# Kernel optimization log

Measured on AMD Instinct MI355X. Metric: run time of the kernel, lower is better.

## Reference

```python
import jax, jax.numpy as jnp
import numpy as np

K = 9          # kernel_size
PAD = 4        # padding
N_OUT, C_IN = 32, 32


def setup_inputs() -> dict:
    key = jax.random.key(0)
    k1, k2, k3, k4, k5 = jax.random.split(key, 5)
    x = jax.random.normal(k1, (16, C_IN, 192, 192), jnp.float32)
    sx = jax.random.uniform(k2, (N_OUT, C_IN), jnp.float32, 0.2, 4.0)
    sy = jax.random.uniform(k3, (N_OUT, C_IN), jnp.float32, 0.2, 4.0)
    th = jax.random.uniform(k4, (N_OUT, C_IN), jnp.float32, 0.0, 2.0 * np.pi)
    weight = jnp.stack([sx, sy, th], axis=-1)          # [N, C, 3]
    bias = jax.random.normal(k5, (N_OUT,), jnp.float32) * 0.01
    return {"x": x, "weight": weight, "bias": bias}


def _gaussian_kernels(weight, k):
    # weight: [N, C, 3] -> normalized anisotropic Gaussian kernels [N, C, k, k]
    sx, sy = weight[..., 0], weight[..., 1]
    rad = weight[..., 2] / 180.0 * jnp.pi          # matches theta/180*pi in source
    c, s = jnp.cos(rad), jnp.sin(rad)
    sx2, sy2 = sx * sx, sy * sy
    # Sigma = U diag(sx^2, sy^2) U^T, U = [[c,-s],[s,c]] -> Sigma = [[a,b],[b,d]]
    a = c * c * sx2 + s * s * sy2
    b = c * s * (sx2 - sy2)
    d = s * s * sx2 + c * c * sy2
    det = a * d - b * b
    ia, ib, id_ = d / det, -b / det, a / det       # closed-form 2x2 inverse
    ax = jnp.arange(k, dtype=jnp.float32) - k // 2
    xx = ax[None, :]                               # x varies along columns
    yy = ax[:, None]                               # y varies along rows
    # quadratic form: ia*x^2 + 2*ib*x*y + id*y^2, broadcast to [N, C, k, k]
    q = (ia[..., None, None] * (xx * xx)
         + 2.0 * ib[..., None, None] * (xx * yy)
         + id_[..., None, None] * (yy * yy))
    ker = jnp.exp(-0.5 * q)
    return ker / jnp.sum(ker, axis=(-2, -1), keepdims=True)


def reference(x, weight, bias):
    w = _gaussian_kernels(weight, K)               # [N, C, K, K]
    out = jax.lax.conv_general_dilated(
        x, w, window_strides=(1, 1), padding=[(PAD, PAD), (PAD, PAD)],
        dimension_numbers=("NCHW", "OIHW", "NCHW"))
    return out + bias[None, :, None, None]
```

## Files before the change

kernel.cpp:

```cpp
#include <hip/hip_runtime.h>
#include <stdint.h>

#define H 192
#define W 192
#define CIN 32
#define NOUT 32
#define NB 16
#define PADI 4

#define HT 16
#define WTL 16
#define RROWS 24
#define RCOLS 24

typedef __attribute__((ext_vector_type(8))) short bf16x8;
typedef __attribute__((ext_vector_type(4))) float f32x4;

__device__ __forceinline__ unsigned short f2bf(float f) {
    union { float f; unsigned int u; } v; v.f = f;
    unsigned int r = v.u + 0x7fffu + ((v.u >> 16) & 1u);
    return (unsigned short)(r >> 16);
}

__device__ __forceinline__ unsigned int cvtpk_bf16(float lo, float hi) {
    unsigned int r;
    asm("v_cvt_pk_bf16_f32 %0, %1, %2" : "=v"(r) : "v"(lo), "v"(hi));
    return r;
}

__global__ void genw_kernel(const float* __restrict__ wp, unsigned short* __restrict__ W2g) {
    const int b = blockIdx.x;
    const int o = b >> 5;
    const int i = b & 31;
    const int t = threadIdx.x;

    float sx = wp[b * 3 + 0], sy = wp[b * 3 + 1], th = wp[b * 3 + 2];
    float rad = th / 180.0f * 3.14159265358979323846f;
    float co = cosf(rad), si = sinf(rad);
    float sx2 = sx * sx, sy2 = sy * sy;
    float a = co * co * sx2 + si * si * sy2;
    float bb = co * si * (sx2 - sy2);
    float d = si * si * sx2 + co * co * sy2;
    float det = a * d - bb * bb;
    float ia = d / det, ib = -bb / det, idd = a / det;

    const int tap = t;
    float e = 0.0f;
    if (tap < 81) {
        float xx = (float)(tap % 9 - 4);
        float yy = (float)(tap / 9 - 4);
        float q = ia * xx * xx + 2.0f * ib * xx * yy + idd * yy * yy;
        e = expf(-0.5f * q);
    }
    float s = e;
    #pragma unroll
    for (int off = 32; off > 0; off >>= 1) s += __shfl_down(s, off);
    __shared__ float ws[2];
    if ((t & 63) == 0) ws[t >> 6] = s;
    __syncthreads();
    float total = ws[0] + ws[1];

    if (tap < 81) {
        int mt = o >> 4, m = o & 15, quad = i >> 3, j = i & 7;
        W2g[((((mt * 81 + tap) * 4 + quad) * 16 + m) << 3) + j] = f2bf(e / total);
    }
}

__global__ __launch_bounds__(256, 4) void conv_kernel(
    const float* __restrict__ x, const unsigned short* __restrict__ W2g,
    const float* __restrict__ bias, float* __restrict__ out)
{
    __shared__ __align__(16) unsigned short ldsx[4 * RROWS * RCOLS * 8];

    const int t = threadIdx.x;
    const int bid = (blockIdx.x & 7) * 288 + (blockIdx.x >> 3);
    const int wb = bid % (W / WTL);
    const int hb = (bid / (W / WTL)) % (H / HT);
    const int n  = bid / ((W / WTL) * (H / HT));
    const int row0 = hb * HT - PADI;
    const int col0 = wb * WTL - PADI;
    const float* xn = x + (size_t)n * CIN * H * W;

    const int wave = t >> 6;
    const int lane = t & 63;
    const int l15 = lane & 15;
    const int quad4 = lane >> 4;
    const int mt = wave & 1;
    const int rbase = (wave >> 1) * 8;

    float bb[4];
    #pragma unroll
    for (int reg = 0; reg < 4; reg++) bb[reg] = bias[mt * 16 + quad4 * 4 + reg];

    float v[9][8];
    #pragma unroll
    for (int it = 0; it < 9; ++it) {
        int idx = it * 256 + t;
        int w = idx % RCOLS;
        int r = (idx / RCOLS) % RROWS;
        int quad = idx / (RCOLS * RROWS);
        int row = row0 + r, col = col0 + w;
        #pragma unroll
        for (int k = 0; k < 8; k++) v[it][k] = 0.0f;
        if ((unsigned)row < (unsigned)H && (unsigned)col < (unsigned)W) {
            const float* p = xn + ((size_t)(quad * 8) * H + row) * W + col;
            #pragma unroll
            for (int k = 0; k < 8; k++) v[it][k] = p[(size_t)k * H * W];
        }
    }
    #pragma unroll
    for (int it = 0; it < 9; ++it) {
        int idx = it * 256 + t;
        unsigned int d[4];
        #pragma unroll
        for (int k = 0; k < 4; k++)
            d[k] = cvtpk_bf16(v[it][2 * k], v[it][2 * k + 1]);
        *(uint4*)&ldsx[(size_t)idx * 8] = make_uint4(d[0], d[1], d[2], d[3]);
    }

    const bf16x8* __restrict__ Wpt = (const bf16x8*)W2g;

    bf16x8 A[2][9];
    #pragma unroll
    for (int dy = 0; dy < 9; dy++)
        A[0][dy] = Wpt[((mt * 81 + dy * 9 + 0) * 4 + quad4) * 16 + l15];

    __syncthreads();

    f32x4 acc[8];
    #pragma unroll
    for (int i = 0; i < 8; i++)
        acc[i] = (f32x4){bb[0], bb[1], bb[2], bb[3]};

    const unsigned short* bptr = &ldsx[(size_t)(((quad4 * RROWS + rbase) * RCOLS) + l15) * 8];

    #pragma unroll
    for (int dx = 0; dx < 9; dx++) {
        const int cur = dx & 1, nxt = cur ^ 1;
        if (dx < 8) {
            #pragma unroll
            for (int dy = 0; dy < 9; dy++)
                A[nxt][dy] = Wpt[((mt * 81 + dy * 9 + (dx + 1)) * 4 + quad4) * 16 + l15];
        }
        #pragma unroll
        for (int rr = 0; rr < 16; rr++) {
            const bf16x8 bfrag = *(const bf16x8*)&bptr[(size_t)(rr * RCOLS + dx) * 8];
            #pragma unroll
            for (int dy = 0; dy < 9; dy++) {
                const int orr = rr - dy;
                if (orr >= 0 && orr < 8) {
                    acc[orr] = __builtin_amdgcn_mfma_f32_16x16x32_bf16(
                        A[cur][dy], bfrag, acc[orr], 0, 0, 0);
                }
            }
        }
    }

    float* outn = out + (size_t)n * NOUT * H * W;
    #pragma unroll
    for (int orr = 0; orr < 8; orr++) {
        const int row = hb * HT + rbase + orr;
        const int col = wb * WTL + l15;
        #pragma unroll
        for (int reg = 0; reg < 4; reg++) {
            const int och = mt * 16 + quad4 * 4 + reg;
            outn[((size_t)och * H + row) * W + col] = acc[orr][reg];
        }
    }
}

extern "C" void kernel_launch(void* const* d_in, const int* in_sizes, int n_in,
                              void* d_out, int out_size, void* d_ws, size_t ws_size,
                              hipStream_t stream) {
    const float* x    = (const float*)d_in[0];
    const float* wp   = (const float*)d_in[1];
    const float* bias = (const float*)d_in[2];
    float* out = (float*)d_out;
    unsigned short* W2g = (unsigned short*)d_ws;

    genw_kernel<<<NOUT * CIN, 128, 0, stream>>>(wp, W2g);
    const int blocks = NB * (H / HT) * (W / WTL);
    conv_kernel<<<blocks, 256, 0, stream>>>(x, W2g, bias, out);
}
```

Measured before the change: 188.4 us.

## Widen conv tile to 32 columns, each wave computing both output-channel halves

The spatial tile width is doubled to 32 columns. Each wave now computes all 32 output channels (two accumulator sets) for a 16-column half instead of one 16-channel half, so each LDS B-fragment feeds two MFMAs. This shrinks halo overhead (a 40-column halo for 32 outputs instead of 24 for 16) and halves the number of blocks. Weight prefetch is ping-ponged with explicit buffers and MFMA sections get raised wave priority. The cost is about twice the accumulator and weight registers, with launch bounds lowered to 2 blocks per CU, so occupancy drops.

Result: no change. 189.0 us (+0.3%).

```diff
diff --git a/kernel.cpp b/kernel.cpp
--- a/kernel.cpp
+++ b/kernel.cpp
@@ -9,9 +9,10 @@
 #define PADI 4
 
 #define HT 16
-#define WTL 16
-#define RROWS 24
-#define RCOLS 24
+#define WT2 32
+#define RR2 24
+#define RC2 40
+#define NT (NB * (H / HT) * (W / WT2))
 
 typedef __attribute__((ext_vector_type(8))) short bf16x8;
 typedef __attribute__((ext_vector_type(4))) float f32x4;
@@ -66,39 +67,42 @@
     }
 }
 
-__global__ __launch_bounds__(256, 4) void conv_kernel(
+__global__ __launch_bounds__(256, 2) void conv_kernel(
     const float* __restrict__ x, const unsigned short* __restrict__ W2g,
     const float* __restrict__ bias, float* __restrict__ out)
 {
-    __shared__ __align__(16) unsigned short ldsx[4 * RROWS * RCOLS * 8];
+    __shared__ __align__(16) unsigned short ldsx[4 * RR2 * RC2 * 8];
 
     const int t = threadIdx.x;
-    const int bid = (blockIdx.x & 7) * 288 + (blockIdx.x >> 3);
-    const int wb = bid % (W / WTL);
-    const int hb = (bid / (W / WTL)) % (H / HT);
-    const int n  = bid / ((W / WTL) * (H / HT));
+    const int bid = (blockIdx.x & 7) * 144 + (blockIdx.x >> 3);
+    const int wb = bid % (W / WT2);
+    const int hb = (bid / (W / WT2)) % (H / HT);
+    const int n  = bid / ((W / WT2) * (H / HT));
     const int row0 = hb * HT - PADI;
-    const int col0 = wb * WTL - PADI;
+    const int col0 = wb * WT2 - PADI;
     const float* xn = x + (size_t)n * CIN * H * W;
 
     const int wave = t >> 6;
     const int lane = t & 63;
     const int l15 = lane & 15;
     const int quad4 = lane >> 4;
-    const int mt = wave & 1;
+    const int ch2 = wave & 1;
     const int rbase = (wave >> 1) * 8;
 
-    float bb[4];
-    #pragma unroll
-    for (int reg = 0; reg < 4; reg++) bb[reg] = bias[mt * 16 + quad4 * 4 + reg];
-
-    float v[9][8];
-    #pragma unroll
-    for (int it = 0; it < 9; ++it) {
+    float bb0[4], bb1[4];
+    #pragma unroll
+    for (int reg = 0; reg < 4; reg++) {
+        bb0[reg] = bias[quad4 * 4 + reg];
+        bb1[reg] = bias[16 + quad4 * 4 + reg];
+    }
+
+    float v[15][8];
+    #pragma unroll
+    for (int it = 0; it < 15; ++it) {
         int idx = it * 256 + t;
-        int w = idx % RCOLS;
-        int r = (idx / RCOLS) % RROWS;
-        int quad = idx / (RCOLS * RROWS);
+        int w = idx % RC2;
+        int r = (idx / RC2) % RR2;
+        int quad = idx / (RC2 * RR2);
         int row = row0 + r, col = col0 + w;
         #pragma unroll
         for (int k = 0; k < 8; k++) v[it][k] = 0.0f;
@@ -109,7 +113,7 @@
         }
     }
     #pragma unroll
-    for (int it = 0; it < 9; ++it) {
+    for (int it = 0; it < 15; ++it) {
         int idx = it * 256 + t;
         unsigned int d[4];
         #pragma unroll
@@ -120,51 +124,69 @@
 
     const bf16x8* __restrict__ Wpt = (const bf16x8*)W2g;
 
-    bf16x8 A[2][9];
-    #pragma unroll
-    for (int dy = 0; dy < 9; dy++)
-        A[0][dy] = Wpt[((mt * 81 + dy * 9 + 0) * 4 + quad4) * 16 + l15];
+    bf16x8 Aa0[9], Aa1[9], Ab0[9], Ab1[9];
+    #pragma unroll
+    for (int dy = 0; dy < 9; dy++) {
+        Aa0[dy] = Wpt[((dy * 9 + 0) * 4 + quad4) * 16 + l15];
+        Aa1[dy] = Wpt[((81 + dy * 9 + 0) * 4 + quad4) * 16 + l15];
+    }
 
     __syncthreads();
 
-    f32x4 acc[8];
-    #pragma unroll
-    for (int i = 0; i < 8; i++)
-        acc[i] = (f32x4){bb[0], bb[1], bb[2], bb[3]};
-
-    const unsigned short* bptr = &ldsx[(size_t)(((quad4 * RROWS + rbase) * RCOLS) + l15) * 8];
-
-    #pragma unroll
-    for (int dx = 0; dx < 9; dx++) {
-        const int cur = dx & 1, nxt = cur ^ 1;
-        if (dx < 8) {
-            #pragma unroll
-            for (int dy = 0; dy < 9; dy++)
-                A[nxt][dy] = Wpt[((mt * 81 + dy * 9 + (dx + 1)) * 4 + quad4) * 16 + l15];
-        }
-        #pragma unroll
-        for (int rr = 0; rr < 16; rr++) {
-            const bf16x8 bfrag = *(const bf16x8*)&bptr[(size_t)(rr * RCOLS + dx) * 8];
-            #pragma unroll
-            for (int dy = 0; dy < 9; dy++) {
-                const int orr = rr - dy;
-                if (orr >= 0 && orr < 8) {
-                    acc[orr] = __builtin_amdgcn_mfma_f32_16x16x32_bf16(
-                        A[cur][dy], bfrag, acc[orr], 0, 0, 0);
-                }
-            }
-        }
-    }
+    f32x4 acc0[8], acc1[8];
+    #pragma unroll
+    for (int i = 0; i < 8; i++) {
+        acc0[i] = (f32x4){bb0[0], bb0[1], bb0[2], bb0[3]};
+        acc1[i] = (f32x4){bb1[0], bb1[1], bb1[2], bb1[3]};
+    }
+
+    const unsigned short* bptr =
+        &ldsx[(size_t)(((quad4 * RR2 + rbase) * RC2) + ch2 * 16 + l15) * 8];
+
+#define DX_BODY(Ac0, Ac1, An0, An1, dxv, pfv, DO_PF)                          \
+    {                                                                          \
+        if (DO_PF) {                                                           \
+            _Pragma("unroll")                                                  \
+            for (int dy = 0; dy < 9; dy++) {                                   \
+                An0[dy] = Wpt[((dy * 9 + (pfv)) * 4 + quad4) * 16 + l15];      \
+                An1[dy] = Wpt[((81 + dy * 9 + (pfv)) * 4 + quad4) * 16 + l15]; \
+            }                                                                  \
+        }                                                                      \
+        __builtin_amdgcn_s_setprio(1);                                         \
+        _Pragma("unroll")                                                      \
+        for (int rr = 0; rr < 16; rr++) {                                      \
+            const bf16x8 bfrag =                                               \
+                *(const bf16x8*)&bptr[(size_t)(rr * RC2 + (dxv)) * 8];         \
+            _Pragma("unroll")                                                  \
+            for (int dy = 0; dy < 9; dy++) {                                   \
+                const int orr = rr - dy;                                       \
+                if (orr >= 0 && orr < 8) {                                     \
+                    acc0[orr] = __builtin_amdgcn_mfma_f32_16x16x32_bf16(       \
+                        Ac0[dy], bfrag, acc0[orr], 0, 0, 0);                   \
+                    acc1[orr] = __builtin_amdgcn_mfma_f32_16x16x32_bf16(       \
+                        Ac1[dy], bfrag, acc1[orr], 0, 0, 0);                   \
+                }                                                              \
+            }                                                                  \
+        }                                                                      \
+        __builtin_amdgcn_s_setprio(0);                                         \
+    }
+
+    for (int dx = 0; dx < 8; dx += 2) {
+        DX_BODY(Aa0, Aa1, Ab0, Ab1, dx, dx + 1, true);
+        DX_BODY(Ab0, Ab1, Aa0, Aa1, dx + 1, dx + 2, true);
+    }
+    DX_BODY(Aa0, Aa1, Ab0, Ab1, 8, 0, false);
+#undef DX_BODY
 
     float* outn = out + (size_t)n * NOUT * H * W;
+    const int col = wb * WT2 + ch2 * 16 + l15;
     #pragma unroll
     for (int orr = 0; orr < 8; orr++) {
         const int row = hb * HT + rbase + orr;
-        const int col = wb * WTL + l15;
         #pragma unroll
         for (int reg = 0; reg < 4; reg++) {
-            const int och = mt * 16 + quad4 * 4 + reg;
-            outn[((size_t)och * H + row) * W + col] = acc[orr][reg];
+            outn[((size_t)(quad4 * 4 + reg) * H + row) * W + col] = acc0[orr][reg];
+            outn[((size_t)(16 + quad4 * 4 + reg) * H + row) * W + col] = acc1[orr][reg];
         }
     }
 }
@@ -179,6 +201,5 @@
     unsigned short* W2g = (unsigned short*)d_ws;
 
     genw_kernel<<<NOUT * CIN, 128, 0, stream>>>(wp, W2g);
-    const int blocks = NB * (H / HT) * (W / WTL);
-    conv_kernel<<<blocks, 256, 0, stream>>>(x, W2g, bias, out);
-}
+    conv_kernel<<<NT, 256, 0, stream>>>(x, W2g, bias, out);
+}
```

## Make conv kernel persistent with register-staged prefetch of next tile

Applied to the files above, without the earlier changes.

Replaces the one-tile-per-block grid with a persistent grid of 512 blocks, each handling 4-5 consecutive tiles within one XCD's range. The global loads for the next tile are issued into registers after the LDS sync, so they overlap the current tile's MFMA work. MFMA sections also raise wave priority via s_setprio, and the launch bound drops to 2 blocks per CU. The volatile pointer on x forces loads to be issued in order and stops the compiler from moving them. This may limit scheduling, and the lower occupancy and extra register pressure could cost more than the overlap gains.

After: 396.1 us. 110% more time.

```diff
diff --git a/kernel.cpp b/kernel.cpp
--- a/kernel.cpp
+++ b/kernel.cpp
@@ -12,6 +12,9 @@
 #define WTL 16
 #define RROWS 24
 #define RCOLS 24
+#define NTILES (NB * (H / HT) * (W / WTL))
+#define NBLK 512
+#define TPX (NTILES / 8)
 
 typedef __attribute__((ext_vector_type(8))) short bf16x8;
 typedef __attribute__((ext_vector_type(4))) float f32x4;
@@ -66,20 +69,18 @@
     }
 }
 
-__global__ __launch_bounds__(256, 4) void conv_kernel(
+__global__ __launch_bounds__(256, 2) void conv_kernel(
     const float* __restrict__ x, const unsigned short* __restrict__ W2g,
     const float* __restrict__ bias, float* __restrict__ out)
 {
     __shared__ __align__(16) unsigned short ldsx[4 * RROWS * RCOLS * 8];
 
     const int t = threadIdx.x;
-    const int bid = (blockIdx.x & 7) * 288 + (blockIdx.x >> 3);
-    const int wb = bid % (W / WTL);
-    const int hb = (bid / (W / WTL)) % (H / HT);
-    const int n  = bid / ((W / WTL) * (H / HT));
-    const int row0 = hb * HT - PADI;
-    const int col0 = wb * WTL - PADI;
-    const float* xn = x + (size_t)n * CIN * H * W;
+    const int xcd  = blockIdx.x & 7;
+    const int slot = blockIdx.x >> 3;
+    int t0, cnt;
+    if (slot < 32) { cnt = 5; t0 = xcd * TPX + slot * 5; }
+    else           { cnt = 4; t0 = xcd * TPX + 160 + (slot - 32) * 4; }
 
     const int wave = t >> 6;
     const int lane = t & 63;
@@ -88,85 +89,114 @@
     const int mt = wave & 1;
     const int rbase = (wave >> 1) * 8;
 
+    int gw[9], gr[9], gq[9];
+    #pragma unroll
+    for (int it = 0; it < 9; ++it) {
+        const int idx = it * 256 + t;
+        gw[it] = idx % RCOLS;
+        gr[it] = (idx / RCOLS) % RROWS;
+        gq[it] = idx / (RCOLS * RROWS);
+    }
+
+    const bf16x8* __restrict__ Wpt = (const bf16x8*)W2g;
     float bb[4];
     #pragma unroll
     for (int reg = 0; reg < 4; reg++) bb[reg] = bias[mt * 16 + quad4 * 4 + reg];
 
+    const volatile float* xv = x;
     float v[9][8];
-    #pragma unroll
-    for (int it = 0; it < 9; ++it) {
-        int idx = it * 256 + t;
-        int w = idx % RCOLS;
-        int r = (idx / RCOLS) % RROWS;
-        int quad = idx / (RCOLS * RROWS);
-        int row = row0 + r, col = col0 + w;
-        #pragma unroll
-        for (int k = 0; k < 8; k++) v[it][k] = 0.0f;
-        if ((unsigned)row < (unsigned)H && (unsigned)col < (unsigned)W) {
-            const float* p = xn + ((size_t)(quad * 8) * H + row) * W + col;
+
+#define STAGE(gt)                                                              \
+    {                                                                          \
+        const int wb_ = (gt) % 12, hb_ = ((gt) / 12) % 12, n_ = (gt) / 144;    \
+        const int row0_ = hb_ * HT - PADI, col0_ = wb_ * WTL - PADI;           \
+        const volatile float* xn_ = xv + (size_t)n_ * CIN * H * W;             \
+        _Pragma("unroll")                                                      \
+        for (int it = 0; it < 9; ++it) {                                       \
+            const int row = row0_ + gr[it], col = col0_ + gw[it];              \
+            _Pragma("unroll")                                                  \
+            for (int k = 0; k < 8; k++) v[it][k] = 0.0f;                       \
+            if ((unsigned)row < (unsigned)H && (unsigned)col < (unsigned)W) {  \
+                const volatile float* p =                                      \
+                    xn_ + ((size_t)(gq[it] * 8) * H + row) * W + col;          \
+                _Pragma("unroll")                                              \
+                for (int k = 0; k < 8; k++) v[it][k] = p[(size_t)k * H * W];   \
+            }                                                                  \
+        }                                                                      \
+    }
+
+    STAGE(t0);
+
+    for (int i = 0; i < cnt; ++i) {
+        const int g = t0 + i;
+        const int wb = g % 12, hb = (g / 12) % 12, n = g / 144;
+
+        #pragma unroll
+        for (int it = 0; it < 9; ++it) {
+            const int idx = it * 256 + t;
+            unsigned int d[4];
             #pragma unroll
-            for (int k = 0; k < 8; k++) v[it][k] = p[(size_t)k * H * W];
+            for (int k = 0; k < 4; k++)
+                d[k] = cvtpk_bf16(v[it][2 * k], v[it][2 * k + 1]);
+            *(uint4*)&ldsx[(size_t)idx * 8] = make_uint4(d[0], d[1], d[2], d[3]);
         }
-    }
-    #pragma unroll
-    for (int it = 0; it < 9; ++it) {
-        int idx = it * 256 + t;
-        unsigned int d[4];
-        #pragma unroll
-        for (int k = 0; k < 4; k++)
-            d[k] = cvtpk_bf16(v[it][2 * k], v[it][2 * k + 1]);
-        *(uint4*)&ldsx[(size_t)idx * 8] = make_uint4(d[0], d[1], d[2], d[3]);
-    }
-
-    const bf16x8* __restrict__ Wpt = (const bf16x8*)W2g;
-
-    bf16x8 A[2][9];
-    #pragma unroll
-    for (int dy = 0; dy < 9; dy++)
-        A[0][dy] = Wpt[((mt * 81 + dy * 9 + 0) * 4 + quad4) * 16 + l15];
-
-    __syncthreads();
-
-    f32x4 acc[8];
-    #pragma unroll
-    for (int i = 0; i < 8; i++)
-        acc[i] = (f32x4){bb[0], bb[1], bb[2], bb[3]};
-
-    const unsigned short* bptr = &ldsx[(size_t)(((quad4 * RROWS + rbase) * RCOLS) + l15) * 8];
-
-    #pragma unroll
-    for (int dx = 0; dx < 9; dx++) {
-        const int cur = dx & 1, nxt = cur ^ 1;
-        if (dx < 8) {
+
+        bf16x8 A[2][9];
+        #pragma unroll
+        for (int dy = 0; dy < 9; dy++)
+            A[0][dy] = Wpt[((mt * 81 + dy * 9 + 0) * 4 + quad4) * 16 + l15];
+
+        __syncthreads();
+
+        if (i + 1 < cnt) STAGE(g + 1);
+
+        f32x4 acc[8];
+        #pragma unroll
+        for (int j = 0; j < 8; j++)
+            acc[j] = (f32x4){bb[0], bb[1], bb[2], bb[3]};
+
+        const unsigned short* bptr =
+            &ldsx[(size_t)(((quad4 * RROWS + rbase) * RCOLS) + l15) * 8];
+
+        #pragma unroll
+        for (int dx = 0; dx < 9; dx++) {
+            const int cur = dx & 1, nxt = cur ^ 1;
+            if (dx < 8) {
+                #pragma unroll
+                for (int dy = 0; dy < 9; dy++)
+                    A[nxt][dy] = Wpt[((mt * 81 + dy * 9 + (dx + 1)) * 4 + quad4) * 16 + l15];
+            }
+            __builtin_amdgcn_s_setprio(1);
             #pragma unroll
-            for (int dy = 0; dy < 9; dy++)
-                A[nxt][dy] = Wpt[((mt * 81 + dy * 9 + (dx + 1)) * 4 + quad4) * 16 + l15];
-        }
-        #pragma unroll
-        for (int rr = 0; rr < 16; rr++) {
-            const bf16x8 bfrag = *(const bf16x8*)&bptr[(size_t)(rr * RCOLS + dx) * 8];
-            #pragma unroll
-            for (int dy = 0; dy < 9; dy++) {
-                const int orr = rr - dy;
-                if (orr >= 0 && orr < 8) {
-                    acc[orr] = __builtin_amdgcn_mfma_f32_16x16x32_bf16(
-                        A[cur][dy], bfrag, acc[orr], 0, 0, 0);
+            for (int rr = 0; rr < 16; rr++) {
+                const bf16x8 bfrag = *(const bf16x8*)&bptr[(size_t)(rr * RCOLS + dx) * 8];
+                #pragma unroll
+                for (int dy = 0; dy < 9; dy++) {
+                    const int orr = rr - dy;
+                    if (orr >= 0 && orr < 8) {
+                        acc[orr] = __builtin_amdgcn_mfma_f32_16x16x32_bf16(
+                            A[cur][dy], bfrag, acc[orr], 0, 0, 0);
+                    }
                 }
             }
+            __builtin_amdgcn_s_setprio(0);
         }
-    }
-
-    float* outn = out + (size_t)n * NOUT * H * W;
-    #pragma unroll
-    for (int orr = 0; orr < 8; orr++) {
-        const int row = hb * HT + rbase + orr;
-        const int col = wb * WTL + l15;
-        #pragma unroll
-        for (int reg = 0; reg < 4; reg++) {
-            const int och = mt * 16 + quad4 * 4 + reg;
-            outn[((size_t)och * H + row) * W + col] = acc[orr][reg];
+
+        float* outn = out + (size_t)n * NOUT * H * W;
+        #pragma unroll
+        for (int orr = 0; orr < 8; orr++) {
+            const int row = hb * HT + rbase + orr;
+            const int col = wb * WTL + l15;
+            #pragma unroll
+            for (int reg = 0; reg < 4; reg++) {
+                const int och = mt * 16 + quad4 * 4 + reg;
+                outn[((size_t)och * H + row) * W + col] = acc[orr][reg];
+            }
         }
-    }
+
+        __syncthreads();
+    }
+#undef STAGE
 }
 
 extern "C" void kernel_launch(void* const* d_in, const int* in_sizes, int n_in,
@@ -179,6 +209,5 @@
     unsigned short* W2g = (unsigned short*)d_ws;
 
     genw_kernel<<<NOUT * CIN, 128, 0, stream>>>(wp, W2g);
-    const int blocks = NB * (H / HT) * (W / WTL);
-    conv_kernel<<<blocks, 256, 0, stream>>>(x, W2g, bias, out);
-}
+    conv_kernel<<<NBLK, 256, 0, stream>>>(x, W2g, bias, out);
+}
```
